# Performance work log

Hardware: AMD Instinct MI355X
Metric: run time of the kernel (lower is better)

The kernel has to match this reference:

```python
import jax, jax.numpy as jnp
import numpy as np

# Configuration (mirrors BatchWiseSimCLR with batch_size=64, mask_size=512, temperature=0.5)
B = 64          # args.batch_size
TWO_B = 2 * B   # 128
K = 256         # number of chunks of size 2B in x (and in x_pair); K + K = mask_size
MS = 512        # mask_size = K + K'
D = 256         # projection feature dim
TEMP = 0.5      # temperature
EPS = 1e-8      # torch F.cosine_similarity eps


def setup_inputs() -> dict:
    key = jax.random.key(0)
    k1, k2 = jax.random.split(key)
    x = jax.random.normal(k1, (TWO_B * K, D), dtype=jnp.float32)
    x_pair = jax.random.normal(k2, (TWO_B * K, D), dtype=jnp.float32)
    return {"x": x, "x_pair": x_pair}


def _cosine_sim(a, b):
    # torch.F.cosine_similarity: clamp each norm at eps
    na = jnp.maximum(jnp.linalg.norm(a, axis=-1), EPS)
    nb = jnp.maximum(jnp.linalg.norm(b, axis=-1), EPS)
    return jnp.sum(a * b, axis=-1) / (na * nb)


def reference(x, x_pair):
    # ---- positive loss ----
    # x.split(x_pair.shape[0]) yields a single chunk here (N == M), matching
    # the torch loop which keeps only the last chunk's loss.
    n_positives = x.shape[0] / x_pair.shape[0]  # == 1.0
    loss_pos = jnp.mean(_cosine_sim(x, x_pair) / TEMP / n_positives)

    # ---- negative loss ----
    # torch: cat of chunks of size 2B along new dim 1 -> element [r, i, :] = x[i*2B + r]
    x_r = x.reshape(K, TWO_B, D).transpose(1, 0, 2)        # [2B, K, D]
    xp_r = x_pair.reshape(K, TWO_B, D).transpose(1, 0, 2)  # [2B, K, D]
    z = jnp.concatenate([x_r, xp_r], axis=1)               # [2B, MS, D]

    zn = z / jnp.maximum(jnp.linalg.norm(z, axis=-1, keepdims=True), EPS)
    sim = jnp.einsum('bid,bjd->bij', zn, zn) / TEMP        # [2B, MS, MS]

    # mask diagonal (self-similarity) per batch element, logsumexp over the
    # remaining MS-1 entries of each row
    eye = jnp.eye(MS, dtype=bool)
    masked = jnp.where(eye[None, :, :], -jnp.inf, sim)
    loss_neg = jnp.mean(jax.scipy.special.logsumexp(masked, axis=2))

    return loss_neg - loss_pos
```

## Files before the change

### kernel.cpp

```cpp
#include <hip/hip_runtime.h>


#define TWO_B   128
#define MS      512
#define DDIM    256
#define NROWS   32768
#define TEMP_INV 2.0f
#define EPSN     1e-8f
#define SQRT2   1.41421356237f

typedef __attribute__((ext_vector_type(8))) short  short8;
typedef __attribute__((ext_vector_type(4))) float  f32x4;

__device__ __forceinline__ unsigned short f2bf(float f) {
  union { float f; unsigned u; } c; c.f = f;
  unsigned r = (c.u + 0x7FFFu + ((c.u >> 16) & 1u)) >> 16;
  return (unsigned short)r;
}

#define GLDS16(gp, lp)                                                         \
  __builtin_amdgcn_global_load_lds(                                            \
      (const __attribute__((address_space(1))) unsigned int*)(gp),             \
      (__attribute__((address_space(3))) unsigned int*)(lp), 16, 0, 0)


__global__ __launch_bounds__(256) void k_norm_f(
    const float* __restrict__ x, const float* __restrict__ xp,
    unsigned short* __restrict__ zn) {
  const int wid = threadIdx.x >> 6, lane = threadIdx.x & 63;
  #pragma unroll
  for (int itr = 0; itr < 4; ++itr) {
    const int r = itr * 8192 + blockIdx.x * 4 + wid;
    const int b = r & 127, i = r >> 7;
    const float4 a = ((const float4*)(x  + (size_t)r * DDIM))[lane];
    const float4 p = ((const float4*)(xp + (size_t)r * DDIM))[lane];
    float sxx = a.x*a.x + a.y*a.y + a.z*a.z + a.w*a.w;
    float spp = p.x*p.x + p.y*p.y + p.z*p.z + p.w*p.w;
    #pragma unroll
    for (int m = 1; m < 64; m <<= 1) {
      sxx += __shfl_xor(sxx, m);
      spp += __shfl_xor(spp, m);
    }
    const float inx = SQRT2 / fmaxf(sqrtf(sxx), EPSN);
    const float inp = SQRT2 / fmaxf(sqrtf(spp), EPSN);
    const int us = (lane * 4) ^ ((i & 7) << 3);
    ushort4 ox, op;
    ox.x = f2bf(a.x * inx); ox.y = f2bf(a.y * inx);
    ox.z = f2bf(a.z * inx); ox.w = f2bf(a.w * inx);
    op.x = f2bf(p.x * inp); op.y = f2bf(p.y * inp);
    op.z = f2bf(p.z * inp); op.w = f2bf(p.w * inp);
    *(ushort4*)(zn + ((size_t)(b * MS + i)       * DDIM) + us) = ox;
    *(ushort4*)(zn + ((size_t)(b * MS + 256 + i) * DDIM) + us) = op;
  }
}

__device__ __forceinline__ void stage_b32(const unsigned short* g,
                                          unsigned short* d, int wid, int lane) {
  #pragma unroll
  for (int s = 0; s < 4; ++s) {
    const int c = wid * 4 + s;
    GLDS16(g + c * 512 + lane * 8, d + c * 512);
  }
}

__global__ __launch_bounds__(256, 3) void k_neg_f4(
    const unsigned short* __restrict__ zn,
    float* __restrict__ negp, float* __restrict__ posn) {
  __shared__ __align__(16) unsigned short sh[3][32 * 256];
  const int b  = blockIdx.x;
  const int it = blockIdx.y;
  const int lane = threadIdx.x & 63, wid = threadIdx.x >> 6;
  const int l15 = lane & 15, hi = lane >> 4;
  const int ri = hi << 2;

  short8 av[2][8];
  #pragma unroll
  for (int rb = 0; rb < 2; ++rb) {
    const int arow = it * 128 + wid * 32 + rb * 16 + l15;
    const unsigned short* gr = zn + (size_t)(b * MS + arow) * DDIM;
    const int swz = (arow & 7) << 3;
    #pragma unroll
    for (int kk = 0; kk < 8; ++kk) {
      const int col = kk * 32 + (hi << 3);
      av[rb][kk] = *(const short8*)(gr + (col ^ swz));
    }
  }

  const unsigned short* gB = zn + (size_t)b * MS * DDIM;
  stage_b32(gB,         sh[0], wid, lane);
  stage_b32(gB + 8192,  sh[1], wid, lane);
  stage_b32(gB + 16384, sh[2], wid, lane);

  float rowacc[2][4] = {{0,0,0,0},{0,0,0,0}};
  float posl = 0.0f;

  #pragma unroll
  for (int jt = 0; jt < 16; ++jt) {
    if (jt <= 13)      asm volatile("s_waitcnt vmcnt(8)" ::: "memory");
    else if (jt == 14) asm volatile("s_waitcnt vmcnt(4)" ::: "memory");
    else               asm volatile("s_waitcnt vmcnt(0)" ::: "memory");
    __builtin_amdgcn_sched_barrier(0);
    __builtin_amdgcn_s_barrier();
    __builtin_amdgcn_sched_barrier(0);

    const unsigned short* Bsrc = sh[jt % 3];
    f32x4 acc[2][2];
    acc[0][0] = (f32x4){0,0,0,0}; acc[0][1] = (f32x4){0,0,0,0};
    acc[1][0] = (f32x4){0,0,0,0}; acc[1][1] = (f32x4){0,0,0,0};

    __builtin_amdgcn_s_setprio(1);
    #pragma unroll
    for (int kk = 0; kk < 8; ++kk) {
      const int col = kk * 32 + (hi << 3);
      #pragma unroll
      for (int ni = 0; ni < 2; ++ni) {
        const int br = ni * 16 + l15;
        const short8 bv = *(const short8*)(Bsrc + br * 256 + (col ^ ((br & 7) << 3)));
        acc[0][ni] = __builtin_amdgcn_mfma_f32_16x16x32_bf16(av[0][kk], bv, acc[0][ni], 0, 0, 0);
        acc[1][ni] = __builtin_amdgcn_mfma_f32_16x16x32_bf16(av[1][kk], bv, acc[1][ni], 0, 0, 0);
      }
    }
    __builtin_amdgcn_s_setprio(0);

    __builtin_amdgcn_sched_barrier(0);
    __builtin_amdgcn_s_barrier();
    __builtin_amdgcn_sched_barrier(0);
    if (jt < 13) stage_b32(gB + (size_t)(jt + 3) * 8192, sh[jt % 3], wid, lane);

    #pragma unroll
    for (int rb = 0; rb < 2; ++rb) {
      const int tb = it * 128 + wid * 32 + rb * 16;
      #pragma unroll
      for (int ni = 0; ni < 2; ++ni) {
        const int jtb = jt * 32 + ni * 16;
        const bool dtile = (jtb == tb);
        const bool ptile = (jtb == tb + 256);
        #pragma unroll
        for (int r2 = 0; r2 < 4; ++r2) {
          const float s = acc[rb][ni][r2];
          float e = __expf(s);
          if (dtile && l15 == ri + r2) e = 0.0f;
          rowacc[rb][r2] += e;
          if (ptile && l15 == ri + r2) posl += s;
        }
      }
    }
  }

  float partial = 0.0f;
  #pragma unroll
  for (int rb = 0; rb < 2; ++rb)
    #pragma unroll
    for (int r2 = 0; r2 < 4; ++r2) {
      float v = rowacc[rb][r2];
      v += __shfl_xor(v, 1); v += __shfl_xor(v, 2);
      v += __shfl_xor(v, 4); v += __shfl_xor(v, 8);
      partial += __logf(v);
    }
  partial += __shfl_xor(partial, 16);
  partial += __shfl_xor(partial, 32);
  #pragma unroll
  for (int m = 1; m < 64; m <<= 1) posl += __shfl_xor(posl, m);

  __shared__ float sn[4], sp2[4];
  if (lane == 0) { sn[wid] = partial; sp2[wid] = posl; }
  __syncthreads();
  if (threadIdx.x == 0) {
    const int bid = blockIdx.y * TWO_B + blockIdx.x;
    negp[bid] = sn[0] + sn[1] + sn[2] + sn[3];
    posn[bid] = sp2[0] + sp2[1] + sp2[2] + sp2[3];
  }
}

__global__ __launch_bounds__(256) void k_fin_f(
    const float* __restrict__ posn, const float* __restrict__ negp,
    float* __restrict__ out) {
  const int t = threadIdx.x, wid = t >> 6, lane = t & 63;
  float p = posn[t] + posn[t + 256];
  float n = negp[t] + negp[t + 256];
  #pragma unroll
  for (int m = 1; m < 64; m <<= 1) { p += __shfl_xor(p, m); n += __shfl_xor(n, m); }
  __shared__ float sp[4], sq[4];
  if (lane == 0) { sp[wid] = p; sq[wid] = n; }
  __syncthreads();
  if (t == 0) {
    const float pt = sp[0] + sp[1] + sp[2] + sp[3];
    const float nt = sq[0] + sq[1] + sq[2] + sq[3];
    out[0] = nt * (1.0f / 65536.0f) - pt * (1.0f / 32768.0f);
  }
}


__global__ __launch_bounds__(256) void k_norm(
    const float* __restrict__ x, const float* __restrict__ xp,
    float* __restrict__ invx, float* __restrict__ invp, float* __restrict__ posp) {
  const int wid = threadIdx.x >> 6, lane = threadIdx.x & 63;
  float posl = 0.0f;
  #pragma unroll
  for (int itr = 0; itr < 8; ++itr) {
    const int r = itr * 4096 + blockIdx.x * 4 + wid;
    const float4 a = ((const float4*)(x  + (size_t)r * DDIM))[lane];
    const float4 b = ((const float4*)(xp + (size_t)r * DDIM))[lane];
    float sxx = a.x*a.x + a.y*a.y + a.z*a.z + a.w*a.w;
    float spp = b.x*b.x + b.y*b.y + b.z*b.z + b.w*b.w;
    float sxp = a.x*b.x + a.y*b.y + a.z*b.z + a.w*b.w;
    #pragma unroll
    for (int m = 1; m < 64; m <<= 1) {
      sxx += __shfl_xor(sxx, m);
      spp += __shfl_xor(spp, m);
      sxp += __shfl_xor(sxp, m);
    }
    const float inx = 1.0f / fmaxf(sqrtf(sxx), EPSN);
    const float inp = 1.0f / fmaxf(sqrtf(spp), EPSN);
    if (lane == 0) {
      invx[r] = inx; invp[r] = inp;
      posl += sxp * inx * inp * TEMP_INV;
    }
  }
  __shared__ float cp[4];
  if (lane == 0) cp[wid] = posl;
  __syncthreads();
  if (threadIdx.x == 0) posp[blockIdx.x] = cp[0] + cp[1] + cp[2] + cp[3];
}

__device__ __forceinline__ void stage_tile(
    unsigned short* dst, const float* __restrict__ x, const float* __restrict__ xp,
    const float* __restrict__ invx, const float* __restrict__ invp, int b, int tilebase) {
  const int t = threadIdx.x;
  const bool isp = (tilebase >= 256);
  const float* src = isp ? xp : x;
  const float* inv = isp ? invp : invx;
  const int base_i = isp ? (tilebase - 256) : tilebase;
  #pragma unroll
  for (int s = 0; s < 16; ++s) {
    const int u   = s * 256 + t;
    const int row = u >> 6, c4 = u & 63;
    const int g   = (base_i + row) * TWO_B + b;
    const float4 v = *(const float4*)(src + (size_t)g * DDIM + c4 * 4);
    const float sc = inv[g];
    ushort4 o;
    o.x = f2bf(v.x * sc); o.y = f2bf(v.y * sc);
    o.z = f2bf(v.z * sc); o.w = f2bf(v.w * sc);
    *(ushort4*)(dst + row * 256 + ((c4 * 4) ^ ((row & 7) << 3))) = o;
  }
}

__global__ __launch_bounds__(256, 2) void k_neg(
    const float* __restrict__ x, const float* __restrict__ xp,
    const float* __restrict__ invx, const float* __restrict__ invp,
    float* __restrict__ negp) {
  __shared__ __align__(16) unsigned short As[64 * 256];
  __shared__ __align__(16) unsigned short Bs[64 * 256];
  const int b  = blockIdx.x;
  const int it = blockIdx.y;
  const int lane = threadIdx.x & 63, wid = threadIdx.x >> 6;

  stage_tile(As, x, xp, invx, invp, b, it * 64);
  float rowacc[4] = {0, 0, 0, 0};

  for (int jt = 0; jt < 8; ++jt) {
    __syncthreads();
    stage_tile(Bs, x, xp, invx, invp, b, jt * 64);
    __syncthreads();

    f32x4 acc[4] = {{0,0,0,0},{0,0,0,0},{0,0,0,0},{0,0,0,0}};
    #pragma unroll
    for (int kk = 0; kk < 8; ++kk) {
      const int col = kk * 32 + ((lane >> 4) << 3);
      const int ar  = wid * 16 + (lane & 15);
      const short8 av = *(const short8*)(As + ar * 256 + (col ^ ((ar & 7) << 3)));
      #pragma unroll
      for (int ni = 0; ni < 4; ++ni) {
        const int br = ni * 16 + (lane & 15);
        const short8 bv = *(const short8*)(Bs + br * 256 + (col ^ ((br & 7) << 3)));
        acc[ni] = __builtin_amdgcn_mfma_f32_16x16x32_bf16(av, bv, acc[ni], 0, 0, 0);
      }
    }
    const int igb = it * 64 + wid * 16 + ((lane >> 4) << 2);
    #pragma unroll
    for (int ni = 0; ni < 4; ++ni) {
      const int jg = jt * 64 + ni * 16 + (lane & 15);
      #pragma unroll
      for (int r2 = 0; r2 < 4; ++r2) {
        const float s = acc[ni][r2] * TEMP_INV;
        rowacc[r2] += ((igb + r2) == jg) ? 0.0f : __expf(s);
      }
    }
  }

  float partial = 0.0f;
  #pragma unroll
  for (int r2 = 0; r2 < 4; ++r2) {
    float v = rowacc[r2];
    v += __shfl_xor(v, 1); v += __shfl_xor(v, 2);
    v += __shfl_xor(v, 4); v += __shfl_xor(v, 8);
    partial += __logf(v);
  }
  partial += __shfl_xor(partial, 16);
  partial += __shfl_xor(partial, 32);

  __shared__ float sn[4];
  if (lane == 0) sn[wid] = partial;
  __syncthreads();
  if (threadIdx.x == 0)
    negp[blockIdx.y * TWO_B + blockIdx.x] = sn[0] + sn[1] + sn[2] + sn[3];
}

__global__ __launch_bounds__(256) void k_fin(
    const float* __restrict__ posp, const float* __restrict__ negp,
    float* __restrict__ out) {
  const int t = threadIdx.x, wid = t >> 6, lane = t & 63;
  const float4 p4 = ((const float4*)posp)[t];
  const float4 n4 = ((const float4*)negp)[t];
  float p = p4.x + p4.y + p4.z + p4.w;
  float n = n4.x + n4.y + n4.z + n4.w;
  #pragma unroll
  for (int m = 1; m < 64; m <<= 1) { p += __shfl_xor(p, m); n += __shfl_xor(n, m); }
  __shared__ float sp[4], sq[4];
  if (lane == 0) { sp[wid] = p; sq[wid] = n; }
  __syncthreads();
  if (t == 0) {
    const float pt = sp[0] + sp[1] + sp[2] + sp[3];
    const float nt = sq[0] + sq[1] + sq[2] + sq[3];
    out[0] = nt * (1.0f / 65536.0f) - pt * (1.0f / 32768.0f);
  }
}

extern "C" void kernel_launch(void* const* d_in, const int* in_sizes, int n_in,
                              void* d_out, int out_size, void* d_ws, size_t ws_size,
                              hipStream_t stream) {
  const float* x  = (const float*)d_in[0];
  const float* xp = (const float*)d_in[1];
  float* wsf = (float*)d_ws;
  float* out = (float*)d_out;

  const size_t need_fast = 4096 + (size_t)65536 * DDIM * 2;
  if (ws_size >= need_fast) {
    float* negp = wsf;
    float* posn = wsf + 512;
    unsigned short* zn = (unsigned short*)(wsf + 1024);
    k_norm_f<<<2048, 256, 0, stream>>>(x, xp, zn);
    k_neg_f4<<<dim3(TWO_B, 4), 256, 0, stream>>>(zn, negp, posn);
    k_fin_f<<<1, 256, 0, stream>>>(posn, negp, out);
  } else {
    float* invx = wsf;
    float* invp = wsf + NROWS;
    float* posp = wsf + 2 * NROWS;
    float* negp = wsf + 2 * NROWS + 1024;
    k_norm<<<1024, 256, 0, stream>>>(x, xp, invx, invp, posp);
    k_neg<<<dim3(TWO_B, 8), 256, 0, stream>>>(x, xp, invx, invp, negp);
    k_fin<<<1, 256, 0, stream>>>(posp, negp, out);
  }
}
```

Baseline: 120.5 us.

## Replace LDS-staged B tiles with direct register double-buffered global loads

The normalization kernel now writes the bf16 normalized rows in a 16-row tiled layout instead of a swizzled row-major layout. The similarity kernel drops the triple-buffered LDS staging (global_load_lds plus waitcnt and barriers) and loads each B tile straight from global or L2 into registers, double-buffered across two 16-column tiles. The aim is to remove LDS traffic and barrier overhead. In exchange, all four waves redundantly fetch the same B data from cache, and register pressure and load latency exposure go up.

```diff
diff --git a/kernel.cpp b/kernel.cpp
--- a/kernel.cpp
+++ b/kernel.cpp
@@ -18,15 +18,10 @@
   return (unsigned short)r;
 }
 
-#define GLDS16(gp, lp)                                                         \
-  __builtin_amdgcn_global_load_lds(                                            \
-      (const __attribute__((address_space(1))) unsigned int*)(gp),             \
-      (__attribute__((address_space(3))) unsigned int*)(lp), 16, 0, 0)
-
 
 __global__ __launch_bounds__(256) void k_norm_f(
     const float* __restrict__ x, const float* __restrict__ xp,
-    unsigned short* __restrict__ zn) {
+    unsigned short* __restrict__ zn2) {
   const int wid = threadIdx.x >> 6, lane = threadIdx.x & 63;
   #pragma unroll
   for (int itr = 0; itr < 4; ++itr) {
@@ -43,109 +38,85 @@
     }
     const float inx = SQRT2 / fmaxf(sqrtf(sxx), EPSN);
     const float inp = SQRT2 / fmaxf(sqrtf(spp), EPSN);
-    const int us = (lane * 4) ^ ((i & 7) << 3);
     ushort4 ox, op;
     ox.x = f2bf(a.x * inx); ox.y = f2bf(a.y * inx);
     ox.z = f2bf(a.z * inx); ox.w = f2bf(a.w * inx);
     op.x = f2bf(p.x * inp); op.y = f2bf(p.y * inp);
     op.z = f2bf(p.z * inp); op.w = f2bf(p.w * inp);
-    *(ushort4*)(zn + ((size_t)(b * MS + i)       * DDIM) + us) = ox;
-    *(ushort4*)(zn + ((size_t)(b * MS + 256 + i) * DDIM) + us) = op;
-  }
-}
-
-__device__ __forceinline__ void stage_b32(const unsigned short* g,
-                                          unsigned short* d, int wid, int lane) {
-  #pragma unroll
-  for (int s = 0; s < 4; ++s) {
-    const int c = wid * 4 + s;
-    GLDS16(g + c * 512 + lane * 8, d + c * 512);
-  }
-}
-
-__global__ __launch_bounds__(256, 3) void k_neg_f4(
-    const unsigned short* __restrict__ zn,
+    const int jx = i, jp = 256 + i;
+    const size_t base = (size_t)b * 131072;
+    *(ushort4*)(zn2 + base + (jx >> 4) * 4096 + (jx & 15) * 256 + lane * 4) = ox;
+    *(ushort4*)(zn2 + base + (jp >> 4) * 4096 + (jp & 15) * 256 + lane * 4) = op;
+  }
+}
+
+__global__ __launch_bounds__(256, 3) void k_neg_f5(
+    const unsigned short* __restrict__ zn2,
     float* __restrict__ negp, float* __restrict__ posn) {
-  __shared__ __align__(16) unsigned short sh[3][32 * 256];
   const int b  = blockIdx.x;
   const int it = blockIdx.y;
   const int lane = threadIdx.x & 63, wid = threadIdx.x >> 6;
   const int l15 = lane & 15, hi = lane >> 4;
   const int ri = hi << 2;
+  const unsigned short* zb = zn2 + (size_t)b * 131072;
+  const int fr = l15 * 256 + hi * 8;
 
   short8 av[2][8];
   #pragma unroll
   for (int rb = 0; rb < 2; ++rb) {
-    const int arow = it * 128 + wid * 32 + rb * 16 + l15;
-    const unsigned short* gr = zn + (size_t)(b * MS + arow) * DDIM;
-    const int swz = (arow & 7) << 3;
-    #pragma unroll
-    for (int kk = 0; kk < 8; ++kk) {
-      const int col = kk * 32 + (hi << 3);
-      av[rb][kk] = *(const short8*)(gr + (col ^ swz));
-    }
-  }
-
-  const unsigned short* gB = zn + (size_t)b * MS * DDIM;
-  stage_b32(gB,         sh[0], wid, lane);
-  stage_b32(gB + 8192,  sh[1], wid, lane);
-  stage_b32(gB + 16384, sh[2], wid, lane);
+    const unsigned short* gt = zb + (it * 8 + wid * 2 + rb) * 4096 + fr;
+    #pragma unroll
+    for (int kk = 0; kk < 8; ++kk)
+      av[rb][kk] = *(const short8*)(gt + kk * 32);
+  }
 
   float rowacc[2][4] = {{0,0,0,0},{0,0,0,0}};
   float posl = 0.0f;
-
-  #pragma unroll
-  for (int jt = 0; jt < 16; ++jt) {
-    if (jt <= 13)      asm volatile("s_waitcnt vmcnt(8)" ::: "memory");
-    else if (jt == 14) asm volatile("s_waitcnt vmcnt(4)" ::: "memory");
-    else               asm volatile("s_waitcnt vmcnt(0)" ::: "memory");
-    __builtin_amdgcn_sched_barrier(0);
+  const int tb0 = it * 128 + wid * 32;
+
+  #define LOADB(BV, BT)                                                        \
+    {                                                                          \
+      const unsigned short* gt = zb + (BT) * 4096 + fr;                        \
+      _Pragma("unroll")                                                        \
+      for (int kk = 0; kk < 8; ++kk) (BV)[kk] = *(const short8*)(gt + kk * 32);\
+    }
+
+  #define TILE_STEP(BV, BT)                                                    \
+    {                                                                          \
+      f32x4 a0 = {0, 0, 0, 0}, a1 = {0, 0, 0, 0};                              \
+      _Pragma("unroll")                                                        \
+      for (int kk = 0; kk < 8; ++kk) {                                         \
+        a0 = __builtin_amdgcn_mfma_f32_16x16x32_bf16(av[0][kk], (BV)[kk], a0, 0, 0, 0); \
+        a1 = __builtin_amdgcn_mfma_f32_16x16x32_bf16(av[1][kk], (BV)[kk], a1, 0, 0, 0); \
+      }                                                                        \
+      const int jtb = (BT) * 16;                                               \
+      _Pragma("unroll")                                                        \
+      for (int rb = 0; rb < 2; ++rb) {                                         \
+        const int tb = tb0 + rb * 16;                                          \
+        const bool dtile = (jtb == tb);                      \
+        const bool ptile = (jtb == tb + 256);                \
+        _Pragma("unroll")                                                      \
+        for (int r2 = 0; r2 < 4; ++r2) {                                       \
+          const float s = rb ? a1[r2] : a0[r2];      \
+          float e = __expf(s);                                                 \
+          if (dtile && l15 == ri + r2) e = 0.0f;                               \
+          rowacc[rb][r2] += e;                                                 \
+          if (ptile && l15 == ri + r2) posl += s;                              \
+        }                                                                      \
+      }                                                                        \
+    }
+
+  short8 bva[8], bvb[8];
+  LOADB(bva, 0);
+  for (int bt = 0; bt < 32; bt += 2) {
+    LOADB(bvb, bt + 1);
+    TILE_STEP(bva, bt);
+    if (bt + 2 < 32) LOADB(bva, bt + 2);
+    TILE_STEP(bvb, bt + 1);
     __builtin_amdgcn_s_barrier();
-    __builtin_amdgcn_sched_barrier(0);
-
-    const unsigned short* Bsrc = sh[jt % 3];
-    f32x4 acc[2][2];
-    acc[0][0] = (f32x4){0,0,0,0}; acc[0][1] = (f32x4){0,0,0,0};
-    acc[1][0] = (f32x4){0,0,0,0}; acc[1][1] = (f32x4){0,0,0,0};
-
-    __builtin_amdgcn_s_setprio(1);
-    #pragma unroll
-    for (int kk = 0; kk < 8; ++kk) {
-      const int col = kk * 32 + (hi << 3);
-      #pragma unroll
-      for (int ni = 0; ni < 2; ++ni) {
-        const int br = ni * 16 + l15;
-        const short8 bv = *(const short8*)(Bsrc + br * 256 + (col ^ ((br & 7) << 3)));
-        acc[0][ni] = __builtin_amdgcn_mfma_f32_16x16x32_bf16(av[0][kk], bv, acc[0][ni], 0, 0, 0);
-        acc[1][ni] = __builtin_amdgcn_mfma_f32_16x16x32_bf16(av[1][kk], bv, acc[1][ni], 0, 0, 0);
-      }
-    }
-    __builtin_amdgcn_s_setprio(0);
-
-    __builtin_amdgcn_sched_barrier(0);
-    __builtin_amdgcn_s_barrier();
-    __builtin_amdgcn_sched_barrier(0);
-    if (jt < 13) stage_b32(gB + (size_t)(jt + 3) * 8192, sh[jt % 3], wid, lane);
-
-    #pragma unroll
-    for (int rb = 0; rb < 2; ++rb) {
-      const int tb = it * 128 + wid * 32 + rb * 16;
-      #pragma unroll
-      for (int ni = 0; ni < 2; ++ni) {
-        const int jtb = jt * 32 + ni * 16;
-        const bool dtile = (jtb == tb);
-        const bool ptile = (jtb == tb + 256);
-        #pragma unroll
-        for (int r2 = 0; r2 < 4; ++r2) {
-          const float s = acc[rb][ni][r2];
-          float e = __expf(s);
-          if (dtile && l15 == ri + r2) e = 0.0f;
-          rowacc[rb][r2] += e;
-          if (ptile && l15 == ri + r2) posl += s;
-        }
-      }
-    }
-  }
+  }
+  #undef LOADB
+  #undef TILE_STEP
 
   float partial = 0.0f;
   #pragma unroll
@@ -338,9 +309,9 @@
   if (ws_size >= need_fast) {
     float* negp = wsf;
     float* posn = wsf + 512;
-    unsigned short* zn = (unsigned short*)(wsf + 1024);
-    k_norm_f<<<2048, 256, 0, stream>>>(x, xp, zn);
-    k_neg_f4<<<dim3(TWO_B, 4), 256, 0, stream>>>(zn, negp, posn);
+    unsigned short* zn2 = (unsigned short*)(wsf + 1024);
+    k_norm_f<<<2048, 256, 0, stream>>>(x, xp, zn2);
+    k_neg_f5<<<dim3(TWO_B, 4), 256, 0, stream>>>(zn2, negp, posn);
     k_fin_f<<<1, 256, 0, stream>>>(posn, negp, out);
   } else {
     float* invx = wsf;
```

Result: slower. 161.6 us (+34.1%).
